# Performance work log

Hardware: AMD Instinct MI355X
Metric: run time of the kernel (lower is better)

The kernel has to match this reference:

```python
import jax, jax.numpy as jnp
import numpy as np

N = 5
Z = 20


def _linear_params(key, din, dout, scale=0.02):
    kw, kb = jax.random.split(key)
    W = jax.random.normal(kw, (din, dout), dtype=jnp.float32) * scale
    b = jax.random.normal(kb, (dout,), dtype=jnp.float32) * scale
    return W, b


def setup_inputs() -> dict:
    key = jax.random.key(0)
    ks = jax.random.split(key, 10)
    B = 32768
    x = jax.random.uniform(ks[0], (B, 784), dtype=jnp.float32)
    u = jax.random.uniform(ks[1], (B,), dtype=jnp.float32)
    eps = jax.random.normal(ks[2], (B, Z), dtype=jnp.float32)
    W1, b1 = _linear_params(ks[3], 784, 400)
    Wmu, bmu = _linear_params(ks[4], 400, N * Z)
    WQ, bQ = _linear_params(ks[5], 400, N * Z * Z)
    Wa, ba = _linear_params(ks[6], 400, N)
    We, be = _linear_params(ks[7], 400, N * Z)
    W3, b3 = _linear_params(ks[8], Z, 400)
    W4, b4 = _linear_params(ks[9], 400, 784)
    return {"x": x, "u": u, "eps": eps, "W1": W1, "b1": b1, "Wmu": Wmu, "bmu": bmu,
            "WQ": WQ, "bQ": bQ, "Wa": Wa, "ba": ba, "We": We, "be": be,
            "W3": W3, "b3": b3, "W4": W4, "b4": b4}


def reference(x, u, eps, W1, b1, Wmu, bmu, WQ, bQ, Wa, ba, We, be, W3, b3, W4, b4):
    B = x.shape[0]
    # encode
    h1 = jax.nn.relu(x @ W1 + b1)                                  # [B,400]
    mu = (h1 @ Wmu + bmu).reshape(B, N, Z)                         # [B,N,Z]
    Q = jnp.exp((h1 @ WQ + bQ).reshape(B, N, Z, Z))                # [B,N,Z,Z]
    a = jax.nn.softmax(h1 @ Wa + ba, axis=-1)                      # [B,N]
    eigen = jnp.exp((h1 @ We + be).reshape(B, N, Z))               # [B,N,Z]
    # categorical sampling via inverse CDF on given uniforms u
    cdf = jnp.cumsum(a, axis=-1)                                   # [B,N]
    idx = jnp.argmax(u[:, None] < cdf, axis=-1)                    # [B]
    bidx = jnp.arange(B)
    this_mu = mu[bidx, idx]                                        # [B,Z]
    this_eigen = eigen[bidx, idx]                                  # [B,Z]
    this_Q = Q[bidx, idx]                                          # [B,Z,Z]
    # var = Q diag(eigen) Q^{-1}, fused: (Q * eigen[:,None,:]) @ inv(Q)
    Qinv = jnp.linalg.inv(this_Q)                                  # [B,Z,Z]
    var = jnp.einsum('bij,bj,bjk->bik', this_Q, this_eigen, Qinv)  # [B,Z,Z]
    z = jnp.einsum('bij,bj->bi', var, eps) + this_mu               # [B,Z]
    # decode
    h3 = jax.nn.relu(z @ W3 + b3)
    recon = jax.nn.sigmoid(h3 @ W4 + b4)
    return recon, mu, Q, a, eigen
```

## Files before the change

### kernel.cpp

```cpp
#include <hip/hip_runtime.h>

#define BROWS 32768

typedef _Float16 f16;
typedef __attribute__((ext_vector_type(8))) _Float16 f16x8;
typedef __attribute__((ext_vector_type(8))) short s16x8;
typedef __attribute__((ext_vector_type(4))) float f32x4;

enum { POST_NONE = 0, POST_RELU = 1, POST_EXP = 2, POST_SIG = 3 };

__device__ __forceinline__ unsigned short bf16_rne(float v) {
    unsigned u = __builtin_bit_cast(unsigned, v);
    u += 0x7fffu + ((u >> 16) & 1u);
    return (unsigned short)(u >> 16);
}
__device__ __forceinline__ float bf16_to_f(unsigned short h) {
    unsigned u = ((unsigned)h) << 16;
    return __builtin_bit_cast(float, u);
}
__device__ __forceinline__ float f16b_to_f(unsigned short b) {
    return (float)__builtin_bit_cast(f16, b);
}

template <bool BF16>
__device__ __forceinline__ void split2(float v, unsigned short& hi, unsigned short& lo) {
    if constexpr (BF16) {
        hi = bf16_rne(v);
        lo = bf16_rne((v - bf16_to_f(hi)) * 256.f);
    } else {
        const f16 h = (f16)v;
        hi = __builtin_bit_cast(unsigned short, h);
        lo = __builtin_bit_cast(unsigned short, (f16)((v - (float)h) * 1024.f));
    }
}
template <bool BF16>
__device__ __forceinline__ constexpr float inv_ls() { return BF16 ? (1.f / 256.f) : (1.f / 1024.f); }

template <bool BF16>
__device__ __forceinline__ f32x4 mfma16(s16x8 a, s16x8 b, f32x4 c) {
    if constexpr (BF16)
        return __builtin_amdgcn_mfma_f32_16x16x32_bf16(a, b, c, 0, 0, 0);
    else
        return __builtin_amdgcn_mfma_f32_16x16x32_f16(
            __builtin_bit_cast(f16x8, a), __builtin_bit_cast(f16x8, b), c, 0, 0, 0);
}

__global__ void zero_pad_kernel(unsigned short* p) { p[threadIdx.x] = 0; }

template <bool BF16>
__global__ __launch_bounds__(256) void split_w_kernel(
    const float* __restrict__ W, unsigned short* __restrict__ Wh,
    unsigned short* __restrict__ Wl, int K, int N, int Kpad, int Npad)
{
    const int i = blockIdx.x * 256 + threadIdx.x;
    if (i >= Npad * Kpad) return;
    const int n = i / Kpad, k = i - n * Kpad;
    const float v = (n < N && k < K) ? W[(size_t)k * N + n] : 0.f;
    split2<BF16>(v, Wh[i], Wl[i]);
}

template <int POST, int OUTMODE, bool AINLINE, bool BF16>
__global__ __launch_bounds__(256, 2) void gemm_2plane(
    const float* __restrict__ Af,
    const unsigned short* __restrict__ Ah, const unsigned short* __restrict__ Al,
    const unsigned short* __restrict__ Bh, const unsigned short* __restrict__ Bl,
    const float* __restrict__ bias,
    float* __restrict__ C, unsigned short* __restrict__ Ch, unsigned short* __restrict__ Cl,
    int N, int K, int KPAD, int lda, int ldc)
{
    __shared__ __align__(16) unsigned short As[2][128 * 40];
    __shared__ __align__(16) unsigned short Bs[2][128 * 40];

    const int t = threadIdx.x;
    const int row0 = blockIdx.y * 128;
    const int col0 = blockIdx.x * 128;

    const int wv = t >> 6, lane = t & 63;
    const int wr = (wv & 1) * 64, wc = (wv >> 1) * 64;
    const int l15 = lane & 15, quad = lane >> 4;

    const int sr = t >> 2, sk = (t & 3) * 8;
    const int am = t >> 1, ak0 = (t & 1) * 16;

    f32x4 acc1[4][4] = {};
    f32x4 acc2[4][4] = {};

    for (int kt = 0; kt < KPAD; kt += 32) {
        uint4 b0h, b0l, b1h, b1l;
        {
            const size_t o0 = (size_t)(col0 + sr) * KPAD + kt + sk;
            const size_t o1 = (size_t)(col0 + sr + 64) * KPAD + kt + sk;
            b0h = *(const uint4*)(Bh + o0); b1h = *(const uint4*)(Bh + o1);
            b0l = *(const uint4*)(Bl + o0); b1l = *(const uint4*)(Bl + o1);
        }
        uint4 a0h, a0l, a1h, a1l;
        float av[16];
        if constexpr (AINLINE) {
            const float* Arow = Af + (size_t)(row0 + am) * lda;
            if (kt + ak0 + 16 <= K) {
                const float4* Ap = (const float4*)(Arow + kt + ak0);
#pragma unroll
                for (int j = 0; j < 4; ++j) {
                    float4 q = Ap[j];
                    av[j * 4 + 0] = q.x; av[j * 4 + 1] = q.y;
                    av[j * 4 + 2] = q.z; av[j * 4 + 3] = q.w;
                }
            } else {
#pragma unroll
                for (int i = 0; i < 16; ++i) {
                    int k = kt + ak0 + i;
                    av[i] = (k < K) ? Arow[k] : 0.f;
                }
            }
        } else {
            const size_t o0 = (size_t)(row0 + sr) * lda + kt + sk;
            const size_t o1 = (size_t)(row0 + sr + 64) * lda + kt + sk;
            a0h = *(const uint4*)(Ah + o0); a1h = *(const uint4*)(Ah + o1);
            a0l = *(const uint4*)(Al + o0); a1l = *(const uint4*)(Al + o1);
        }

        __syncthreads();
        if constexpr (AINLINE) {
            union { unsigned short us[16]; uint4 q[2]; } uh, ul;
#pragma unroll
            for (int i = 0; i < 16; ++i)
                split2<BF16>(av[i], uh.us[i], ul.us[i]);
            *(uint4*)&As[0][am * 40 + ak0]     = uh.q[0];
            *(uint4*)&As[0][am * 40 + ak0 + 8] = uh.q[1];
            *(uint4*)&As[1][am * 40 + ak0]     = ul.q[0];
            *(uint4*)&As[1][am * 40 + ak0 + 8] = ul.q[1];
        } else {
            *(uint4*)&As[0][sr * 40 + sk]        = a0h;
            *(uint4*)&As[0][(sr + 64) * 40 + sk] = a1h;
            *(uint4*)&As[1][sr * 40 + sk]        = a0l;
            *(uint4*)&As[1][(sr + 64) * 40 + sk] = a1l;
        }
        *(uint4*)&Bs[0][sr * 40 + sk]        = b0h;
        *(uint4*)&Bs[0][(sr + 64) * 40 + sk] = b1h;
        *(uint4*)&Bs[1][sr * 40 + sk]        = b0l;
        *(uint4*)&Bs[1][(sr + 64) * 40 + sk] = b1l;
        __syncthreads();

        s16x8 af0[4], bf0[4];
#pragma unroll
        for (int i = 0; i < 4; ++i) {
            af0[i] = *(const s16x8*)&As[0][(wr + i * 16 + l15) * 40 + quad * 8];
            bf0[i] = *(const s16x8*)&Bs[0][(wc + i * 16 + l15) * 40 + quad * 8];
        }
#pragma unroll
        for (int mt = 0; mt < 4; ++mt)
#pragma unroll
            for (int nt = 0; nt < 4; ++nt)
                acc1[mt][nt] = mfma16<BF16>(af0[mt], bf0[nt], acc1[mt][nt]);

        {
            s16x8 bf1[4];
#pragma unroll
            for (int i = 0; i < 4; ++i)
                bf1[i] = *(const s16x8*)&Bs[1][(wc + i * 16 + l15) * 40 + quad * 8];
#pragma unroll
            for (int mt = 0; mt < 4; ++mt)
#pragma unroll
                for (int nt = 0; nt < 4; ++nt)
                    acc2[mt][nt] = mfma16<BF16>(af0[mt], bf1[nt], acc2[mt][nt]);
        }
        {
            s16x8 af1[4];
#pragma unroll
            for (int i = 0; i < 4; ++i)
                af1[i] = *(const s16x8*)&As[1][(wr + i * 16 + l15) * 40 + quad * 8];
#pragma unroll
            for (int mt = 0; mt < 4; ++mt)
#pragma unroll
                for (int nt = 0; nt < 4; ++nt)
                    acc2[mt][nt] = mfma16<BF16>(af1[mt], bf0[nt], acc2[mt][nt]);
        }
    }

#pragma unroll
    for (int nt = 0; nt < 4; ++nt) {
        const int col = col0 + wc + nt * 16 + l15;
        if (col < N) {
            const float bval = bias[col];
#pragma unroll
            for (int mt = 0; mt < 4; ++mt) {
                const int rbase = row0 + wr + mt * 16 + quad * 4;
#pragma unroll
                for (int r = 0; r < 4; ++r) {
                    float v = acc1[mt][nt][r] + acc2[mt][nt][r] * inv_ls<BF16>() + bval;
                    if (POST == POST_RELU) v = v > 0.f ? v : 0.f;
                    else if (POST == POST_EXP) v = expf(v);
                    else if (POST == POST_SIG) v = 1.f / (1.f + expf(-v));
                    if (OUTMODE == 0) {
                        C[(size_t)(rbase + r) * ldc + col] = v;
                    } else {
                        split2<BF16>(v, Ch[(size_t)(rbase + r) * ldc + col],
                                        Cl[(size_t)(rbase + r) * ldc + col]);
                    }
                }
            }
        }
    }
}

__global__ __launch_bounds__(256) void a_idx_kernel(
    const unsigned short* __restrict__ h1h, const unsigned short* __restrict__ h1l,
    const float* __restrict__ Wa, const float* __restrict__ ba,
    const float* __restrict__ u, float* __restrict__ a_out,
    int* __restrict__ idx_out)
{
    const int r = blockIdx.x * 4 + (threadIdx.x >> 6);
    const int lane = threadIdx.x & 63;
    const unsigned short* hh = h1h + (size_t)r * 400;
    const unsigned short* hl = h1l + (size_t)r * 400;

    float acc0 = 0.f, acc1 = 0.f, acc2 = 0.f, acc3 = 0.f, acc4 = 0.f;
    for (int k = lane; k < 400; k += 64) {
        const float h = f16b_to_f(hh[k]) + f16b_to_f(hl[k]) * (1.f / 1024.f);
        const float* w = Wa + k * 5;
        acc0 += h * w[0]; acc1 += h * w[1]; acc2 += h * w[2];
        acc3 += h * w[3]; acc4 += h * w[4];
    }
    for (int off = 32; off; off >>= 1) {
        acc0 += __shfl_down(acc0, off);
        acc1 += __shfl_down(acc1, off);
        acc2 += __shfl_down(acc2, off);
        acc3 += __shfl_down(acc3, off);
        acc4 += __shfl_down(acc4, off);
    }
    if (lane == 0) {
        float l[5] = {acc0 + ba[0], acc1 + ba[1], acc2 + ba[2], acc3 + ba[3], acc4 + ba[4]};
        float mx = l[0];
        for (int n = 1; n < 5; ++n) mx = l[n] > mx ? l[n] : mx;
        float e[5], s = 0.f;
        for (int n = 0; n < 5; ++n) { e[n] = expf(l[n] - mx); s += e[n]; }
        const float inv = 1.f / s;
        const float uu = u[r];
        float cdf = 0.f;
        int idx = 0, found = 0;
        for (int n = 0; n < 5; ++n) {
            const float a = e[n] * inv;
            a_out[(size_t)r * 5 + n] = a;
            cdf += a;
            if (!found && uu < cdf) { idx = n; found = 1; }
        }
        idx_out[r] = idx;
    }
}

__global__ __launch_bounds__(256) void solve_kernel(
    const float* __restrict__ mu_o, const float* __restrict__ q_o,
    const float* __restrict__ e_o, const int* __restrict__ idxv,
    const float* __restrict__ eps,
    unsigned short* __restrict__ zh, unsigned short* __restrict__ zl)
{
    __shared__ float LU[4][20][21];
    __shared__ float Qo[4][20][21];
    __shared__ float rhs[4][20];
    __shared__ float wv[4][20];
    __shared__ float ew[4][20];

    const int wsl = threadIdx.x >> 6;
    const int lane = threadIdx.x & 63;
    const int r = blockIdx.x * 4 + wsl;

    const int idx = idxv[r];
    const float* Qp = q_o + (size_t)r * 2000 + idx * 400;
    for (int e = lane; e < 400; e += 64) {
        const float v = Qp[e];
        const int ri = e / 20, ci = e - ri * 20;
        LU[wsl][ri][ci] = v;
        Qo[wsl][ri][ci] = v;
    }
    if (lane < 20) rhs[wsl][lane] = eps[(size_t)r * 20 + lane];
    __syncthreads();

    for (int k = 0; k < 20; ++k) {
        float val = -1.f;
        int ii = k;
        if (lane >= k && lane < 20) { val = fabsf(LU[wsl][lane][k]); ii = lane; }
        for (int off = 32; off; off >>= 1) {
            const float ov = __shfl_down(val, off);
            const int oi = __shfl_down(ii, off);
            if (ov > val) { val = ov; ii = oi; }
        }
        const int piv = __shfl(ii, 0);
        if (piv != k) {
            if (lane < 20) {
                const float t1 = LU[wsl][k][lane], t2 = LU[wsl][piv][lane];
                LU[wsl][k][lane] = t2;
                LU[wsl][piv][lane] = t1;
            } else if (lane == 20) {
                const float t1 = rhs[wsl][k];
                rhs[wsl][k] = rhs[wsl][piv];
                rhs[wsl][piv] = t1;
            }
        }
        __syncthreads();
        const float pv = LU[wsl][k][k];
        if (lane > k && lane < 20) {
            const float m = LU[wsl][lane][k] / pv;
            for (int j = k + 1; j < 20; ++j)
                LU[wsl][lane][j] -= m * LU[wsl][k][j];
            rhs[wsl][lane] -= m * rhs[wsl][k];
        }
        __syncthreads();
    }

    for (int k = 19; k >= 0; --k) {
        const float wk = rhs[wsl][k] / LU[wsl][k][k];
        if (lane == 0) wv[wsl][k] = wk;
        if (lane < k) rhs[wsl][lane] -= LU[wsl][lane][k] * wk;
        __syncthreads();
    }

    if (lane < 20) {
        const float evl = e_o[(size_t)r * 100 + idx * 20 + lane];
        ew[wsl][lane] = evl * wv[wsl][lane];
    }
    __syncthreads();
    float zv = 0.f;
    if (lane < 20) {
        float acc = mu_o[(size_t)r * 100 + idx * 20 + lane];
        for (int j = 0; j < 20; ++j)
            acc += Qo[wsl][lane][j] * ew[wsl][j];
        zv = acc;
    }
    if (lane < 32) {
        split2<true>(zv, zh[(size_t)r * 32 + lane], zl[(size_t)r * 32 + lane]);
    }
}

extern "C" void kernel_launch(void* const* d_in, const int* in_sizes, int n_in,
                              void* d_out, int out_size, void* d_ws, size_t ws_size,
                              hipStream_t stream)
{
    const float* x   = (const float*)d_in[0];
    const float* u   = (const float*)d_in[1];
    const float* eps = (const float*)d_in[2];
    const float* W1  = (const float*)d_in[3];
    const float* b1  = (const float*)d_in[4];
    const float* Wmu = (const float*)d_in[5];
    const float* bmu = (const float*)d_in[6];
    const float* WQ  = (const float*)d_in[7];
    const float* bQ  = (const float*)d_in[8];
    const float* Wa  = (const float*)d_in[9];
    const float* ba  = (const float*)d_in[10];
    const float* We  = (const float*)d_in[11];
    const float* be  = (const float*)d_in[12];
    const float* W3  = (const float*)d_in[13];
    const float* b3  = (const float*)d_in[14];
    const float* W4  = (const float*)d_in[15];
    const float* b4  = (const float*)d_in[16];

    float* out   = (float*)d_out;
    float* recon = out;
    float* mu_o  = out + (size_t)BROWS * 784;
    float* q_o   = mu_o + (size_t)BROWS * 100;
    float* a_o   = q_o + (size_t)BROWS * 2000;
    float* e_o   = a_o + (size_t)BROWS * 5;

    typedef unsigned short us;

    char* p = (char*)d_ws;
    us* h1h = (us*)p; p += (size_t)BROWS * 400 * 2;
    us* h1l = (us*)p; p += (size_t)BROWS * 400 * 2;
    us* pad = (us*)p; p += 64;
    us* W4h = (us*)p; p += (size_t)896 * 416 * 2;
    us* W4l = (us*)p;

    char* rs = (char*)recon;
    us* zh  = (us*)rs; rs += (size_t)BROWS * 32 * 2;
    us* zl  = (us*)rs; rs += (size_t)BROWS * 32 * 2;
    int* idx = (int*)rs; rs += (size_t)BROWS * 4;
    us* W1h = (us*)rs; rs += 512 * 800 * 2;
    us* W1l = (us*)rs; rs += 512 * 800 * 2;
    us* Wmuh = (us*)rs; rs += 128 * 416 * 2;
    us* Wmul = (us*)rs; rs += 128 * 416 * 2;
    us* WQh = (us*)rs; rs += 2048 * 416 * 2;
    us* WQl = (us*)rs; rs += 2048 * 416 * 2;
    us* Weh = (us*)rs; rs += 128 * 416 * 2;
    us* Wel = (us*)rs; rs += 128 * 416 * 2;
    us* W3h = (us*)rs; rs += 512 * 32 * 2;
    us* W3l = (us*)rs;

    const dim3 blk(256);
    const int my = BROWS / 128;
    auto cdiv = [](int a, int b) { return (a + b - 1) / b; };

    zero_pad_kernel<<<1, 32, 0, stream>>>(pad);

    split_w_kernel<false><<<cdiv(512 * 800, 256), blk, 0, stream>>>(W1, W1h, W1l, 784, 400, 800, 512);
    split_w_kernel<false><<<cdiv(128 * 416, 256), blk, 0, stream>>>(Wmu, Wmuh, Wmul, 400, 100, 416, 128);
    split_w_kernel<false><<<cdiv(2048 * 416, 256), blk, 0, stream>>>(WQ, WQh, WQl, 400, 2000, 416, 2048);
    split_w_kernel<false><<<cdiv(128 * 416, 256), blk, 0, stream>>>(We, Weh, Wel, 400, 100, 416, 128);
    split_w_kernel<true><<<cdiv(512 * 32, 256), blk, 0, stream>>>(W3, W3h, W3l, 20, 400, 32, 512);
    split_w_kernel<true><<<cdiv(896 * 416, 256), blk, 0, stream>>>(W4, W4h, W4l, 400, 784, 416, 896);

    gemm_2plane<POST_RELU, 1, true, false><<<dim3(4, my), blk, 0, stream>>>(
        x, nullptr, nullptr, W1h, W1l, b1, nullptr, h1h, h1l, 400, 784, 800, 784, 400);
    gemm_2plane<POST_NONE, 0, false, false><<<dim3(1, my), blk, 0, stream>>>(
        nullptr, h1h, h1l, Wmuh, Wmul, bmu, mu_o, nullptr, nullptr, 100, 400, 416, 400, 100);
    gemm_2plane<POST_EXP, 0, false, false><<<dim3(16, my), blk, 0, stream>>>(
        nullptr, h1h, h1l, WQh, WQl, bQ, q_o, nullptr, nullptr, 2000, 400, 416, 400, 2000);
    gemm_2plane<POST_EXP, 0, false, false><<<dim3(1, my), blk, 0, stream>>>(
        nullptr, h1h, h1l, Weh, Wel, be, e_o, nullptr, nullptr, 100, 400, 416, 400, 100);
    a_idx_kernel<<<BROWS / 4, blk, 0, stream>>>(h1h, h1l, Wa, ba, u, a_o, idx);
    solve_kernel<<<BROWS / 4, blk, 0, stream>>>(mu_o, q_o, e_o, idx, eps, zh, zl);
    gemm_2plane<POST_RELU, 1, false, true><<<dim3(4, my), blk, 0, stream>>>(
        nullptr, zh, zl, W3h, W3l, b3, nullptr, h1h, h1l, 400, 20, 32, 32, 400);
    gemm_2plane<POST_SIG, 0, false, true><<<dim3(7, my), blk, 0, stream>>>(
        nullptr, h1h, h1l, W4h, W4l, b4, recon, nullptr, nullptr, 784, 400, 416, 400, 784);
}
```

Baseline: 1.228 ms.

## Rewrite per-row 20x20 solve as register-resident Gauss-Jordan with wave shuffles

The small linear solve now keeps each matrix row in registers of one lane and does Gauss-Jordan elimination with wave shuffles, replacing the shared-memory LU, its barriers and the serial back-substitution. Pivot search packs the magnitude and lane index into one int for a single-value xor-reduction. The final Q*diag(e)*w product also uses shuffles instead of shared memory. This adds register pressure (about 40 floats per lane) and drops the low 5 mantissa bits when comparing pivots, so tie-breaking between near-equal pivots can change.

```diff
diff --git a/kernel.cpp b/kernel.cpp
--- a/kernel.cpp
+++ b/kernel.cpp
@@ -254,79 +254,77 @@
     const float* __restrict__ eps,
     unsigned short* __restrict__ zh, unsigned short* __restrict__ zl)
 {
-    __shared__ float LU[4][20][21];
-    __shared__ float Qo[4][20][21];
-    __shared__ float rhs[4][20];
-    __shared__ float wv[4][20];
-    __shared__ float ew[4][20];
-
     const int wsl = threadIdx.x >> 6;
     const int lane = threadIdx.x & 63;
     const int r = blockIdx.x * 4 + wsl;
-
     const int idx = idxv[r];
+    const bool rowok = lane < 20;
+
     const float* Qp = q_o + (size_t)r * 2000 + idx * 400;
-    for (int e = lane; e < 400; e += 64) {
-        const float v = Qp[e];
-        const int ri = e / 20, ci = e - ri * 20;
-        LU[wsl][ri][ci] = v;
-        Qo[wsl][ri][ci] = v;
-    }
-    if (lane < 20) rhs[wsl][lane] = eps[(size_t)r * 20 + lane];
-    __syncthreads();
-
+
+    float a[20];
+    float qc[20];
+    float rhs;
+    if (rowok) {
+        const float4* q4 = (const float4*)(Qp + lane * 20);
+#pragma unroll
+        for (int j = 0; j < 5; ++j) {
+            float4 v = q4[j];
+            a[j * 4 + 0] = v.x; a[j * 4 + 1] = v.y;
+            a[j * 4 + 2] = v.z; a[j * 4 + 3] = v.w;
+        }
+#pragma unroll
+        for (int j = 0; j < 20; ++j) qc[j] = a[j];
+        rhs = eps[(size_t)r * 20 + lane];
+    } else {
+#pragma unroll
+        for (int j = 0; j < 20; ++j) { a[j] = 0.f; qc[j] = 0.f; }
+        rhs = 0.f;
+    }
+
+    bool used = !rowok;
+    int mycol = lane;
+
+#pragma unroll
     for (int k = 0; k < 20; ++k) {
-        float val = -1.f;
-        int ii = k;
-        if (lane >= k && lane < 20) { val = fabsf(LU[wsl][lane][k]); ii = lane; }
+        const float cand = used ? -1.f : fabsf(a[k]);
+        int packed = (__builtin_bit_cast(int, cand) & ~31) | lane;
+#pragma unroll
         for (int off = 32; off; off >>= 1) {
-            const float ov = __shfl_down(val, off);
-            const int oi = __shfl_down(ii, off);
-            if (ov > val) { val = ov; ii = oi; }
-        }
-        const int piv = __shfl(ii, 0);
-        if (piv != k) {
-            if (lane < 20) {
-                const float t1 = LU[wsl][k][lane], t2 = LU[wsl][piv][lane];
-                LU[wsl][k][lane] = t2;
-                LU[wsl][piv][lane] = t1;
-            } else if (lane == 20) {
-                const float t1 = rhs[wsl][k];
-                rhs[wsl][k] = rhs[wsl][piv];
-                rhs[wsl][piv] = t1;
-            }
-        }
-        __syncthreads();
-        const float pv = LU[wsl][k][k];
-        if (lane > k && lane < 20) {
-            const float m = LU[wsl][lane][k] / pv;
-            for (int j = k + 1; j < 20; ++j)
-                LU[wsl][lane][j] -= m * LU[wsl][k][j];
-            rhs[wsl][lane] -= m * rhs[wsl][k];
-        }
-        __syncthreads();
-    }
-
-    for (int k = 19; k >= 0; --k) {
-        const float wk = rhs[wsl][k] / LU[wsl][k][k];
-        if (lane == 0) wv[wsl][k] = wk;
-        if (lane < k) rhs[wsl][lane] -= LU[wsl][lane][k] * wk;
-        __syncthreads();
-    }
-
-    if (lane < 20) {
-        const float evl = e_o[(size_t)r * 100 + idx * 20 + lane];
-        ew[wsl][lane] = evl * wv[wsl][lane];
-    }
-    __syncthreads();
-    float zv = 0.f;
-    if (lane < 20) {
-        float acc = mu_o[(size_t)r * 100 + idx * 20 + lane];
-        for (int j = 0; j < 20; ++j)
-            acc += Qo[wsl][lane][j] * ew[wsl][j];
-        zv = acc;
-    }
+            const int o = __shfl_xor(packed, off);
+            packed = o > packed ? o : packed;
+        }
+        const int p = packed & 31;
+        const float pv = __shfl(a[k], p);
+        const float rpv = 1.f / pv;
+        const bool isp = (lane == p);
+        if (isp) { used = true; mycol = k; }
+        const float f = isp ? 0.f : a[k] * rpv;
+        const float s = isp ? rpv : 1.f;
+#pragma unroll
+        for (int j = k + 1; j < 20; ++j) {
+            const float pr = __shfl(a[j], p);
+            a[j] = a[j] * s - f * pr;
+        }
+        const float prr = __shfl(rhs, p);
+        rhs = rhs * s - f * prr;
+    }
+
+    const int wbits = __builtin_amdgcn_ds_permute(
+        mycol << 2, __builtin_bit_cast(int, rhs));
+    const float w_l = __builtin_bit_cast(float, wbits);
+
+    const float e_l  = rowok ? e_o[(size_t)r * 100 + idx * 20 + lane] : 0.f;
+    const float mu_l = rowok ? mu_o[(size_t)r * 100 + idx * 20 + lane] : 0.f;
+    const float ew_l = e_l * w_l;
+
+    float z = mu_l;
+#pragma unroll
+    for (int k = 0; k < 20; ++k)
+        z += qc[k] * __shfl(ew_l, k);
+
     if (lane < 32) {
+        const float zv = rowok ? z : 0.f;
         split2<true>(zv, zh[(size_t)r * 32 + lane], zl[(size_t)r * 32 + lane]);
     }
 }
```

Result: faster. 1.112 ms (-9.4%).
